# Kernel optimization log

Measured on AMD Instinct MI355X. Metric: run time of the kernel, lower is better.

Reference implementation:

```python
import jax, jax.numpy as jnp
import numpy as np

D = 64          # feature dim (in_dim == out_dim)
BS = 16         # graphs per batch
NPG = 4096      # nodes per graph
N = BS * NPG    # total nodes
E = N * 16      # edges (avg degree 16)
L = 2           # total_layer_num
TEMP = 0.6      # RelaxedBernoulli temperature
BN_EPS = 1e-5


def setup_inputs() -> dict:
    key = jax.random.key(0)
    ks = jax.random.split(key, 16)
    s = 0.05
    return {
        "x": jax.random.normal(ks[0], (N, D), jnp.float32),
        "edge_index": jax.random.randint(ks[1], (2, E), 0, N),
        "edge_weight": jax.random.uniform(ks[2], (E,), jnp.float32),
        "batch_item": jnp.repeat(jnp.arange(BS), NPG),
        "bs": BS,
        # per-layer logistic noise for RelaxedBernoulliStraightThrough rsample
        "u_noise": jax.random.uniform(ks[3], (L, E), jnp.float32, 1e-4, 1.0 - 1e-4),
        # edgePredictor (global): Linear(3d,d) -> ReLU -> Linear(d,1)
        "ep_W1": jax.random.normal(ks[4], (3 * D, D), jnp.float32) * s,
        "ep_b1": jnp.zeros((D,), jnp.float32),
        "ep_W2": jax.random.normal(ks[5], (D, 1), jnp.float32) * s,
        "ep_b2": jnp.zeros((1,), jnp.float32),
        "alpha": jax.random.uniform(ks[6], (1,), jnp.float32),  # edge_skip_alpha
        # per-layer GINConv mlp: Linear(d,d) (+ReLU)
        "gin_W": jax.random.normal(ks[7], (L, D, D), jnp.float32) * s,
        "gin_b": jnp.zeros((L, D), jnp.float32),
        # per-layer BatchNorm1d affine params
        "bn_gamma": jnp.ones((L, D), jnp.float32),
        "bn_beta": jnp.zeros((L, D), jnp.float32),
        # mlp_head: Linear(d,d)->ReLU->Linear(d,d)
        "head_W1": jax.random.normal(ks[8], (D, D), jnp.float32) * s,
        "head_b1": jnp.zeros((D,), jnp.float32),
        "head_W2": jax.random.normal(ks[9], (D, D), jnp.float32) * s,
        "head_b2": jnp.zeros((D,), jnp.float32),
    }


def reference(x, edge_index, edge_weight, batch_item, bs, u_noise,
              ep_W1, ep_b1, ep_W2, ep_b2, alpha, gin_W, gin_b,
              bn_gamma, bn_beta, head_W1, head_b1, head_W2, head_b2):
    src, dst = edge_index[0], edge_index[1]
    n_total = x.shape[0]
    centroid = jnp.mean(x.reshape(bs, -1, D), axis=1)  # [bs, D]
    pre_adj = None
    for l in range(L):
        # ---- EdgeUpdate: edge-gather + MLP scorer ----
        nj = x[src]
        ni = x[dst]
        res = (x.reshape(bs, -1, D) - centroid[:, None, :]).reshape(-1, D)
        sim = jnp.concatenate([jnp.abs(ni - nj), res[dst], res[src]], axis=1)  # [E, 3D]
        h = jax.nn.relu(sim @ ep_W1 + ep_b1)
        score = (h @ ep_W2 + ep_b2)[:, 0]  # [E]
        pre_adj = jax.nn.sigmoid(score)
        # RelaxedBernoulliStraightThrough: logits(probs) == score
        g = jnp.log(u_noise[l]) - jnp.log1p(-u_noise[l])
        soft = jax.nn.sigmoid((score + g) / TEMP)
        samp = soft + jax.lax.stop_gradient(jnp.round(soft) - soft)
        edge_weight = alpha * (samp * edge_weight) + (1.0 - alpha) * (samp * pre_adj)
        # ---- NodeUpdate: weighted GINConv (eps=0) + ReLU + BatchNorm ----
        msg = edge_weight[:, None] * x[src]
        aggr = jax.ops.segment_sum(msg, dst, num_segments=n_total)
        xh = jax.nn.relu((x + aggr) @ gin_W[l] + gin_b[l])  # GIN mlp ReLU == outer ReLU
        mu = jnp.mean(xh, axis=0)
        var = jnp.mean((xh - mu) ** 2, axis=0)
        x = bn_gamma[l] * (xh - mu) / jnp.sqrt(var + BN_EPS) + bn_beta[l]
        # ---- SystemUpdate: memory-attention pooling ----
        xm = x.reshape(bs, -1, D)
        att = jax.nn.softmax(jnp.einsum('bnd,bd->bn', xm, centroid), axis=1)
        centroid = jnp.einsum('bn,bnd->bd', att, xm)
    x_loss = jax.nn.relu(x @ head_W1 + head_b1) @ head_W2 + head_b2
    centroid_loss = jax.nn.relu(centroid @ head_W1 + head_b1) @ head_W2 + head_b2
    return (x, edge_weight, centroid, x_loss, centroid_loss, pre_adj)
```

## Files before the change

### kernel.cpp

```cpp
#include <hip/hip_runtime.h>
#include <hip/hip_bf16.h>


#define D 64
#define BSZ 16
#define NPG 4096
#define NN (BSZ * NPG)
#define NE (NN * 16)
#define NL 2
#define NTILE (NE / 64)

#define FIXTH 2e-3f
#define FLAGCAP 65536

#define OUT_X  0u
#define OUT_EW 4194304u
#define OUT_C  5242880u
#define OUT_XL 5243904u
#define OUT_CL 9438208u
#define OUT_PA 9439232u

typedef __attribute__((ext_vector_type(2))) float f32x2;

__device__ __forceinline__ void atomAdd64(double* p, double v) { unsafeAtomicAdd(p, v); }

__global__ __launch_bounds__(256) void k_deg(const int* __restrict__ edst,
                                             int* __restrict__ cnt) {
    int stride = gridDim.x * 256;
    for (int e = blockIdx.x * 256 + threadIdx.x; e < NE; e += stride)
        atomicAdd(&cnt[edst[e]], 1);
}

__global__ __launch_bounds__(256) void k_scan1(const int* __restrict__ cnt,
                                               int* __restrict__ rowptr,
                                               int* __restrict__ bsum) {
    __shared__ int sd[256];
    const int b = blockIdx.x, t = threadIdx.x;
    const int v = cnt[b * 256 + t];
    sd[t] = v;
    __syncthreads();
    for (int off = 1; off < 256; off <<= 1) {
        int tmp = (t >= off) ? sd[t - off] : 0;
        __syncthreads();
        sd[t] += tmp;
        __syncthreads();
    }
    rowptr[b * 256 + t] = sd[t] - v;
    if (t == 255) bsum[b] = sd[255];
}

__global__ __launch_bounds__(256) void k_scan2(int* __restrict__ bsum) {
    __shared__ int sd[256];
    const int t = threadIdx.x;
    const int v = bsum[t];
    sd[t] = v;
    __syncthreads();
    for (int off = 1; off < 256; off <<= 1) {
        int tmp = (t >= off) ? sd[t - off] : 0;
        __syncthreads();
        sd[t] += tmp;
        __syncthreads();
    }
    bsum[t] = sd[t] - v;
}

__global__ __launch_bounds__(256) void k_scan3(const int* __restrict__ bsum,
                                               int* __restrict__ rowptr,
                                               int* __restrict__ cursor) {
    const int i = blockIdx.x * 256 + threadIdx.x;
    const int r = rowptr[i] + bsum[blockIdx.x];
    rowptr[i] = r;
    cursor[i] = r;
    if (i == 0) rowptr[NN] = NE;
}

__global__ __launch_bounds__(256) void k_fill(const int* __restrict__ esrc,
                                              const int* __restrict__ edst,
                                              int* __restrict__ cursor,
                                              int* __restrict__ eord,
                                              int* __restrict__ src_csr,
                                              int* __restrict__ dst_csr) {
    int stride = gridDim.x * 256;
    for (int e = blockIdx.x * 256 + threadIdx.x; e < NE; e += stride) {
        const int d = edst[e];
        int pos = atomicAdd(&cursor[d], 1);
        eord[pos] = e;
        src_csr[pos] = esrc[e];
        dst_csr[pos] = d;
    }
}

__global__ __launch_bounds__(256) void k_centroid0(const float* __restrict__ xin,
                                                   double* __restrict__ c64) {
    const int g = blockIdx.x >> 3, sub = blockIdx.x & 7, tid = threadIdx.x;
    const int r = tid >> 6, f = tid & 63;
    __shared__ double cr[4][D];
    double s = 0.0;
    for (int k = 0; k < NPG / 8 / 4; ++k) {
        size_t n = (size_t)g * NPG + (size_t)(sub * (NPG / 8) + 4 * k + r);
        s += (double)xin[n * D + f];
    }
    cr[r][f] = s;
    __syncthreads();
    if (tid < D)
        atomAdd64(&c64[g * D + tid],
                  (cr[0][tid] + cr[1][tid] + cr[2][tid] + cr[3][tid]) * (1.0 / NPG));
}

__global__ __launch_bounds__(256) void k_qbc(const double* __restrict__ c64,
                                             const float* __restrict__ epW1,
                                             double* __restrict__ qb, double* __restrict__ qc) {
    int gj = blockIdx.x * 256 + threadIdx.x;
    if (gj >= BSZ * D) return;
    int g = gj >> 6, j = gj & 63;
    double sb = 0.0, sc = 0.0;
#pragma unroll
    for (int i = 0; i < D; ++i) {
        double cv = c64[g * D + i];
        sb += cv * (double)epW1[(D + i) * D + j];
        sc += cv * (double)epW1[(2 * D + i) * D + j];
    }
    qb[gj] = sb;
    qc[gj] = sc;
}

template <int LAYER>
__global__ __launch_bounds__(256) void k_P(const float* __restrict__ xin,
                                           const float* __restrict__ x32,
                                           const float* __restrict__ epW1,
                                           const double* __restrict__ qb,
                                           const double* __restrict__ qc,
                                           float* __restrict__ Pb, float* __restrict__ Pc,
                                           double* __restrict__ bnacc) {
    if (blockIdx.x == 0 && threadIdx.x < 128) bnacc[threadIdx.x] = 0.0;
    __shared__ float wb[D * D];
    __shared__ float wc[D * D];
    __shared__ float xrow[4][D];
    int tid = threadIdx.x, w = tid >> 6, j = tid & 63;
    for (int idx = tid; idx < D * D; idx += 256) {
        int i = idx >> 6, c = idx & 63;
        wb[idx] = epW1[(D + i) * D + c];
        wc[idx] = epW1[(2 * D + i) * D + c];
    }
    __syncthreads();
    for (int grp = blockIdx.x; grp < NN / 4; grp += gridDim.x) {
        size_t n = (size_t)grp * 4 + w;
        xrow[w][j] = (LAYER == 0) ? xin[n * D + j] : x32[n * D + j];
        __syncthreads();
        float pb = 0.0f, pc = 0.0f;
#pragma unroll
        for (int i = 0; i < D; ++i) {
            const float xv = xrow[w][i];
            pb += xv * wb[i * D + j];
            pc += xv * wc[i * D + j];
        }
        const int g = (int)(n >> 12);
        Pb[n * D + j] = pb - (float)qb[g * D + j];
        Pc[n * D + j] = pc - (float)qc[g * D + j];
        __syncthreads();
    }
}

template <int LAYER>
__global__ __launch_bounds__(256, 4) void k_edge(const float* __restrict__ xsrc,
                                                 const int* __restrict__ src_csr,
                                                 const int* __restrict__ dst_csr,
                                                 const int* __restrict__ eord,
                                                 const float* __restrict__ ewin,
                                                 float* __restrict__ ew_csr,
                                                 const float* __restrict__ unoise,
                                                 const float* __restrict__ epW1,
                                                 const float* __restrict__ epb1,
                                                 const float* __restrict__ epW2,
                                                 const float* __restrict__ epb2,
                                                 const float* __restrict__ alphap,
                                                 const float* __restrict__ Pb32,
                                                 const float* __restrict__ Pc32,
                                                 int* __restrict__ flagcnt,
                                                 int* __restrict__ flaglist,
                                                 float* __restrict__ out) {
    const int t = threadIdx.x;
    const int tx = t & 15, ty = t >> 4;

    __shared__ __align__(16) float ldsA[64 * 64];
    __shared__ __align__(16) float ldsW[64 * 64];

    for (int idx = t; idx < D * D; idx += 256) {
        ldsW[idx] = epW1[idx];
    }
    float b1f[4], w2f[4];
#pragma unroll
    for (int c = 0; c < 4; ++c) {
        b1f[c] = epb1[4 * tx + c];
        w2f[c] = epW2[4 * tx + c];
    }
    const float b2v = epb2[0];
    const float alpha = alphap[0];
    __syncthreads();

    const int eloc = t >> 2, q = t & 3;

    for (int tile = blockIdx.x; tile < NTILE; tile += gridDim.x) {
        const int base = tile * 64;

        {
            const int pos = base + eloc;
            const int s = src_csr[pos], d = dst_csr[pos];
            const float* rs = xsrc + (size_t)s * D + q * 16;
            const float* rd = xsrc + (size_t)d * D + q * 16;
#pragma unroll
            for (int c = 0; c < 4; ++c) {
                const float4 fd = *(const float4*)(rd + 4 * c);
                const float4 fs = *(const float4*)(rs + 4 * c);
                const int dim = q * 16 + 4 * c;
                ldsA[(dim + 0) * 64 + eloc] = fabsf(fd.x - fs.x);
                ldsA[(dim + 1) * 64 + eloc] = fabsf(fd.y - fs.y);
                ldsA[(dim + 2) * 64 + eloc] = fabsf(fd.z - fs.z);
                ldsA[(dim + 3) * 64 + eloc] = fabsf(fd.w - fs.w);
            }
        }
        __syncthreads();

        f32x2 acc2[4][2];
#pragma unroll
        for (int r = 0; r < 4; ++r)
#pragma unroll
            for (int c = 0; c < 2; ++c) {
                f32x2 z = {0.0f, 0.0f};
                acc2[r][c] = z;
            }

#pragma unroll 4
        for (int k = 0; k < 64; ++k) {
            const float4 af = *(const float4*)&ldsA[k * 64 + 4 * ty];
            const float4 wf = *(const float4*)&ldsW[k * 64 + 4 * tx];
            const f32x2 w01 = {wf.x, wf.y};
            const f32x2 w23 = {wf.z, wf.w};
            const float av[4] = {af.x, af.y, af.z, af.w};
#pragma unroll
            for (int r = 0; r < 4; ++r) {
                const f32x2 avv = {av[r], av[r]};
                acc2[r][0] += avv * w01;
                acc2[r][1] += avv * w23;
            }
        }
        __syncthreads();

        float* sred = ldsA;
#pragma unroll
        for (int r = 0; r < 4; ++r) {
            const int pos = base + 4 * ty + r;
            const int s = src_csr[pos], d = dst_csr[pos];
            const float4 pb = *(const float4*)(Pb32 + (size_t)d * D + 4 * tx);
            const float4 pc = *(const float4*)(Pc32 + (size_t)s * D + 4 * tx);
            float part = 0.0f;
            float h;
            h = acc2[r][0].x + pb.x + pc.x + b1f[0];
            if (h > 0.0f) part += h * w2f[0];
            h = acc2[r][0].y + pb.y + pc.y + b1f[1];
            if (h > 0.0f) part += h * w2f[1];
            h = acc2[r][1].x + pb.z + pc.z + b1f[2];
            if (h > 0.0f) part += h * w2f[2];
            h = acc2[r][1].y + pb.w + pc.w + b1f[3];
            if (h > 0.0f) part += h * w2f[3];
            sred[(4 * ty + r) * 17 + tx] = part;
        }
        __syncthreads();

        if (t < 64) {
            float sc_ = b2v;
#pragma unroll
            for (int i = 0; i < 16; ++i) sc_ += sred[t * 17 + i];
            const int pos = base + t;
            const int e = eord[pos];
            const float u = unoise[(size_t)LAYER * NE + e];
            const float gn = logf(u) - log1pf(-u);
            const float mar = sc_ + gn;
            bool deferred = false;
            if (fabsf(mar) < FIXTH) {
                int slot = atomicAdd(flagcnt, 1);
                if (slot < FLAGCAP) {
                    flaglist[slot] = pos;
                    deferred = true;
                }
            }
            if (!deferred) {
                const float pre = 1.0f / (1.0f + expf(-sc_));
                const bool samp = mar > 0.0f;
                const float ewo = (LAYER == 0) ? ewin[e] : ew_csr[pos];
                const float ewn = samp ? alpha * ewo + (1.0f - alpha) * pre : 0.0f;
                ew_csr[pos] = ewn;
                if (LAYER == NL - 1) {
                    out[OUT_EW + (size_t)e] = ewn;
                    out[OUT_PA + (size_t)e] = pre;
                }
            }
        }
        __syncthreads();
    }
}

template <int LAYER>
__global__ __launch_bounds__(256) void k_fix(const float* __restrict__ xsrc,
                                             const int* __restrict__ src_csr,
                                             const int* __restrict__ dst_csr,
                                             const int* __restrict__ eord,
                                             const float* __restrict__ ewin,
                                             float* __restrict__ ew_csr,
                                             const float* __restrict__ unoise,
                                             const float* __restrict__ epW1,
                                             const float* __restrict__ epb1,
                                             const float* __restrict__ epW2,
                                             const float* __restrict__ epb2,
                                             const float* __restrict__ alphap,
                                             const float* __restrict__ Pb32,
                                             const float* __restrict__ Pc32,
                                             const int* __restrict__ flagcnt,
                                             const int* __restrict__ flaglist,
                                             float* __restrict__ out) {
    const int n = min(flagcnt[0], FLAGCAP);
    __shared__ float dxs[4][D];
    const int w = threadIdx.x >> 6, lane = threadIdx.x & 63;
    const int nw = gridDim.x * 4;
    for (int i = blockIdx.x * 4 + w; i < n; i += nw) {
        const int pos = flaglist[i];
        const int s = src_csr[pos], d = dst_csr[pos];
        dxs[w][lane] = fabsf(xsrc[(size_t)d * D + lane] - xsrc[(size_t)s * D + lane]);
        double h = 0.0;
#pragma unroll
        for (int k = 0; k < D; ++k) h += (double)dxs[w][k] * (double)epW1[k * D + lane];
        h += (double)Pb32[(size_t)d * D + lane] + (double)Pc32[(size_t)s * D + lane] +
             (double)epb1[lane];
        double part = (h > 0.0) ? h * (double)epW2[lane] : 0.0;
#pragma unroll
        for (int off = 32; off; off >>= 1) part += __shfl_xor(part, off);
        if (lane == 0) {
            const double sc_ = part + (double)epb2[0];
            const int e = eord[pos];
            const double u = (double)unoise[(size_t)LAYER * NE + e];
            const double gn = log(u) - log1p(-u);
            const double pre = 1.0 / (1.0 + exp(-sc_));
            const bool samp = (sc_ + gn) > 0.0;
            const double ewo = (LAYER == 0) ? (double)ewin[e] : (double)ew_csr[pos];
            const double alpha = (double)alphap[0];
            const double ewn = samp ? alpha * ewo + (1.0 - alpha) * pre : 0.0;
            ew_csr[pos] = (float)ewn;
            if (LAYER == NL - 1) {
                out[OUT_EW + (size_t)e] = (float)ewn;
                out[OUT_PA + (size_t)e] = (float)pre;
            }
        }
    }
}

template <int LAYER>
__global__ __launch_bounds__(256) void k_nodeup(const float* __restrict__ xsrc,
                                                const float* __restrict__ ew_csr,
                                                const int* __restrict__ src_csr,
                                                const int* __restrict__ rowptr,
                                                const float* __restrict__ ginW,
                                                const float* __restrict__ ginB,
                                                float* __restrict__ xh,
                                                double* __restrict__ bnacc) {
    __shared__ __align__(16) float wgT[D][65];
    __shared__ __align__(16) float rowbuf[4][D];
    __shared__ double bn1[4][D];
    __shared__ double bn2[4][D];
    const int t = threadIdx.x, w = t >> 6, lane = t & 63;
    const int e = lane >> 4, q = lane & 15;
    for (int idx = t; idx < D * D; idx += 256) {
        const int i = idx >> 6, c = idx & 63;
        wgT[c][i] = ginW[LAYER * D * D + idx];
    }
    const float bj = ginB[LAYER * D + lane];
    __syncthreads();
    double s1 = 0.0, s2 = 0.0;
    const int nwaves = gridDim.x * 4;
    for (int n = blockIdx.x * 4 + w; n < NN; n += nwaves) {
        const int rs = rowptr[n], re = rowptr[n + 1];
        const int deg = re - rs;
        const int i0 = rs + ((e < deg) ? e : 0);
        const int i1 = rs + ((4 + e < deg) ? 4 + e : 0);
        const int i2 = rs + ((8 + e < deg) ? 8 + e : 0);
        const int i3 = rs + ((12 + e < deg) ? 12 + e : 0);
        const float w0 = (e < deg) ? ew_csr[i0] : 0.f;
        const float w1 = (4 + e < deg) ? ew_csr[i1] : 0.f;
        const float w2 = (8 + e < deg) ? ew_csr[i2] : 0.f;
        const float w3 = (12 + e < deg) ? ew_csr[i3] : 0.f;
        const int s0 = src_csr[i0], s1_ = src_csr[i1];
        const int s2_ = src_csr[i2], s3_ = src_csr[i3];
        const float4 r0 = *(const float4*)(xsrc + (size_t)s0 * D + 4 * q);
        const float4 r1 = *(const float4*)(xsrc + (size_t)s1_ * D + 4 * q);
        const float4 r2 = *(const float4*)(xsrc + (size_t)s2_ * D + 4 * q);
        const float4 r3 = *(const float4*)(xsrc + (size_t)s3_ * D + 4 * q);
        const float4 rf = *(const float4*)(xsrc + (size_t)n * D + 4 * q);
        f32x2 a01, a23;
        {
            const f32x2 w0v = {w0, w0}, w1v = {w1, w1}, w2v = {w2, w2}, w3v = {w3, w3};
            const f32x2 r0a = {r0.x, r0.y}, r0b = {r0.z, r0.w};
            const f32x2 r1a = {r1.x, r1.y}, r1b = {r1.z, r1.w};
            const f32x2 r2a = {r2.x, r2.y}, r2b = {r2.z, r2.w};
            const f32x2 r3a = {r3.x, r3.y}, r3b = {r3.z, r3.w};
            a01 = w0v * r0a;
            a23 = w0v * r0b;
            a01 += w1v * r1a;
            a23 += w1v * r1b;
            a01 += w2v * r2a;
            a23 += w2v * r2b;
            a01 += w3v * r3a;
            a23 += w3v * r3b;
        }
        for (int k = rs + 16; k < re; k += 4) {
            const int kk = k + e;
            const bool v = kk < re;
            const float wt = v ? ew_csr[kk] : 0.f;
            const int st = src_csr[v ? kk : rs];
            const float4 rt = *(const float4*)(xsrc + (size_t)st * D + 4 * q);
            const f32x2 wtv = {wt, wt};
            const f32x2 rta = {rt.x, rt.y}, rtb = {rt.z, rt.w};
            a01 += wtv * rta;
            a23 += wtv * rtb;
        }
        float a0 = a01.x, a1 = a01.y, a2 = a23.x, a3 = a23.y;
        a0 += __shfl_xor(a0, 16);
        a1 += __shfl_xor(a1, 16);
        a2 += __shfl_xor(a2, 16);
        a3 += __shfl_xor(a3, 16);
        a0 += __shfl_xor(a0, 32);
        a1 += __shfl_xor(a1, 32);
        a2 += __shfl_xor(a2, 32);
        a3 += __shfl_xor(a3, 32);
        if (e == 0) {
            rowbuf[w][4 * q + 0] = a0 + rf.x;
            rowbuf[w][4 * q + 1] = a1 + rf.y;
            rowbuf[w][4 * q + 2] = a2 + rf.z;
            rowbuf[w][4 * q + 3] = a3 + rf.w;
        }
        f32x2 h01 = {bj, 0.0f}, h23 = {0.0f, 0.0f};
#pragma unroll
        for (int ib = 0; ib < 16; ++ib) {
            const float4 rb = *(const float4*)&rowbuf[w][4 * ib];
            const float4 wv = *(const float4*)&wgT[lane][4 * ib];
            const f32x2 ra = {rb.x, rb.y}, rc = {rb.z, rb.w};
            const f32x2 wa = {wv.x, wv.y}, wc = {wv.z, wv.w};
            h01 += ra * wa;
            h23 += rc * wc;
        }
        float h = (h01.x + h01.y) + (h23.x + h23.y);
        h = h > 0.0f ? h : 0.0f;
        xh[(size_t)n * D + lane] = h;
        s1 += (double)h;
        s2 += (double)h * (double)h;
    }
    bn1[w][lane] = s1;
    bn2[w][lane] = s2;
    __syncthreads();
    if (w == 0) {
        atomAdd64(&bnacc[lane], bn1[0][lane] + bn1[1][lane] + bn1[2][lane] + bn1[3][lane]);
        atomAdd64(&bnacc[64 + lane], bn2[0][lane] + bn2[1][lane] + bn2[2][lane] + bn2[3][lane]);
    }
}

__global__ __launch_bounds__(64) void k_bnfin(int layer, const float* __restrict__ gamma,
                                              const float* __restrict__ beta,
                                              const double* __restrict__ bnacc,
                                              double* __restrict__ bnsc) {
    int j = threadIdx.x;
    double mu = bnacc[j] * (1.0 / NN);
    double var = bnacc[64 + j] * (1.0 / NN) - mu * mu;
    double sc = (double)gamma[layer * D + j] / sqrt(var + 1e-5);
    bnsc[j] = sc;
    bnsc[64 + j] = (double)beta[layer * D + j] - mu * sc;
}

template <int LAYER>
__global__ __launch_bounds__(256) void k_att1(const float* __restrict__ xh,
                                              const double* __restrict__ bnsc,
                                              const double* __restrict__ c64,
                                              float* __restrict__ x32,
                                              float* __restrict__ out,
                                              double* __restrict__ sc,
                                              double* __restrict__ bmax) {
    const int blk = blockIdx.x, t = threadIdx.x, w = t >> 6, lane = t & 63;
    const int g = blk >> 6;
    __shared__ double wmax[4];
    const double cj = c64[g * D + lane];
    const double bsc = bnsc[lane], boff = bnsc[64 + lane];
    double locmax = -1e300;
    for (int m = 0; m < 16; ++m) {
        const int n = blk * 64 + w * 16 + m;
        const float v32 = (float)(bsc * (double)xh[(size_t)n * D + lane] + boff);
        x32[(size_t)n * D + lane] = v32;
        if (LAYER == NL - 1) out[OUT_X + (size_t)n * D + lane] = v32;
        double v = (double)v32 * cj;
#pragma unroll
        for (int off = 32; off; off >>= 1) v += __shfl_xor(v, off);
        if (lane == 0) sc[n] = v;
        locmax = fmax(locmax, v);
    }
    if (lane == 0) wmax[w] = locmax;
    __syncthreads();
    if (t == 0) bmax[blk] = fmax(fmax(wmax[0], wmax[1]), fmax(wmax[2], wmax[3]));
}

__global__ __launch_bounds__(64) void k_att2(const double* __restrict__ bmax,
                                             double* __restrict__ mxg,
                                             double* __restrict__ num,
                                             double* __restrict__ den) {
    const int g = blockIdx.x, t = threadIdx.x;
    double m = bmax[g * 64 + t];
#pragma unroll
    for (int off = 32; off; off >>= 1) m = fmax(m, __shfl_xor(m, off));
    if (t == 0) {
        mxg[g] = m;
        den[g] = 0.0;
    }
    num[g * D + t] = 0.0;
}

__global__ __launch_bounds__(256) void k_att3(const float* __restrict__ x32,
                                              const double* __restrict__ sc,
                                              const double* __restrict__ mxg,
                                              double* __restrict__ num,
                                              double* __restrict__ den) {
    const int blk = blockIdx.x, t = threadIdx.x, w = t >> 6, lane = t & 63;
    const int g = blk >> 6;
    __shared__ double cp[4][D];
    __shared__ double wes[4];
    const double mx = mxg[g];
    double accj = 0.0, esum = 0.0;
    for (int m = 0; m < 16; ++m) {
        const int n = blk * 64 + w * 16 + m;
        const double e = exp(sc[n] - mx);
        accj += e * (double)x32[(size_t)n * D + lane];
        esum += e;
    }
    cp[w][lane] = accj;
    if (lane == 0) wes[w] = esum;
    __syncthreads();
    if (t < D) {
        atomAdd64(&num[g * D + t], cp[0][t] + cp[1][t] + cp[2][t] + cp[3][t]);
        if (t == 0) atomAdd64(&den[g], wes[0] + wes[1] + wes[2] + wes[3]);
    }
}

__global__ __launch_bounds__(64) void k_att4(const double* __restrict__ num,
                                             const double* __restrict__ den,
                                             double* __restrict__ c64) {
    const int g = blockIdx.x, t = threadIdx.x;
    c64[g * D + t] = num[g * D + t] / den[g];
}

__global__ __launch_bounds__(256) void k_head(const float* __restrict__ x32,
                                              const double* __restrict__ c64,
                                              const float* __restrict__ hW1,
                                              const float* __restrict__ hb1,
                                              const float* __restrict__ hW2,
                                              const float* __restrict__ hb2,
                                              float* __restrict__ out) {
    __shared__ float w1[D * D];
    __shared__ float w2[D * D];
    __shared__ float xr[4][D];
    __shared__ float hr[4][D];
    int tid = threadIdx.x, w = tid >> 6, j = tid & 63;
    for (int idx = tid; idx < D * D; idx += 256) {
        w1[idx] = hW1[idx];
        w2[idx] = hW2[idx];
    }
    const float b1j = hb1[j];
    const float b2j = hb2[j];
    __syncthreads();
    const int ROWS = NN + BSZ;
    for (int grp = blockIdx.x; grp * 4 < ROWS; grp += gridDim.x) {
        int r = grp * 4 + w;
        bool valid = r < ROWS;
        float xv = 0.f;
        if (valid)
            xv = (r < NN) ? x32[(size_t)r * D + j] : (float)c64[(size_t)(r - NN) * D + j];
        xr[w][j] = xv;
        __syncthreads();
        if (valid) {
            float h = b1j;
#pragma unroll
            for (int i = 0; i < D; ++i) h += xr[w][i] * w1[i * D + j];
            hr[w][j] = h > 0.f ? h : 0.f;
        }
        __syncthreads();
        if (valid) {
            float o = b2j;
#pragma unroll
            for (int i = 0; i < D; ++i) o += hr[w][i] * w2[i * D + j];
            if (r < NN) {
                out[OUT_XL + (size_t)r * D + j] = o;
            } else {
                size_t cr = (size_t)(r - NN) * D + j;
                out[OUT_CL + cr] = o;
                out[OUT_C + cr] = (float)c64[cr];
            }
        }
        __syncthreads();
    }
}

extern "C" void kernel_launch(void* const* d_in, const int* in_sizes, int n_in,
                              void* d_out, int out_size, void* d_ws, size_t ws_size,
                              hipStream_t stream) {
    const float* xin    = (const float*)d_in[0];
    const int*   ei     = (const int*)d_in[1];
    const float* ewin   = (const float*)d_in[2];
    const float* unoise = (const float*)d_in[5];
    const float* epW1   = (const float*)d_in[6];
    const float* epb1   = (const float*)d_in[7];
    const float* epW2   = (const float*)d_in[8];
    const float* epb2   = (const float*)d_in[9];
    const float* alphap = (const float*)d_in[10];
    const float* ginW   = (const float*)d_in[11];
    const float* ginB   = (const float*)d_in[12];
    const float* bng    = (const float*)d_in[13];
    const float* bnb    = (const float*)d_in[14];
    const float* hW1    = (const float*)d_in[15];
    const float* hb1    = (const float*)d_in[16];
    const float* hW2    = (const float*)d_in[17];
    const float* hb2    = (const float*)d_in[18];
    float* out = (float*)d_out;
    const int* esrc = ei;
    const int* edst = ei + NE;

    char* ws = (char*)d_ws;
    const size_t SZ4 = (size_t)NN * D * sizeof(float);
    float* Pb32 = (float*)(ws);
    float* xh32 = Pb32;
    float* Pc32 = (float*)(ws + SZ4);
    float* x32  = (float*)(ws + 2 * SZ4);
    float* ew_csr = (float*)(ws + 3 * SZ4);
    double* sc  = (double*)(ws + 3 * SZ4 + (size_t)NE * 4);
    char*  p    = ws + 3 * SZ4 + (size_t)NE * 4 + (size_t)NN * 8;
    double* c64  = (double*)p;          p += BSZ * D * 8;
    double* qb   = (double*)p;          p += BSZ * D * 8;
    double* qc   = (double*)p;          p += BSZ * D * 8;
    double* bnacc = (double*)p;         p += 128 * 8;
    double* bnsc  = (double*)p;         p += 128 * 8;
    double* bmax  = (double*)p;         p += 1024 * 8;
    double* mxg   = (double*)p;         p += 16 * 8;
    double* num   = (double*)p;         p += BSZ * D * 8;
    double* den   = (double*)p;         p += 16 * 8;
    int* cnt     = (int*)p;             p += (size_t)NN * 4;
    int* rowptr  = (int*)p;             p += (size_t)(NN + 1) * 4 + 4;
    int* cursor  = (int*)p;             p += (size_t)NN * 4;
    int* bsum    = (int*)p;             p += 256 * 4;
    int* eord    = (int*)p;             p += (size_t)NE * 4;
    int* src_csr = (int*)p;             p += (size_t)NE * 4;
    int* dst_csr = (int*)p;             p += (size_t)NE * 4;
    int* flagcnt  = (int*)p;            p += 8;
    int* flaglist = (int*)p;            p += (size_t)FLAGCAP * 4;

    hipMemsetAsync(cnt, 0, (size_t)NN * 4, stream);
    k_deg<<<1024, 256, 0, stream>>>(edst, cnt);
    k_scan1<<<256, 256, 0, stream>>>(cnt, rowptr, bsum);
    k_scan2<<<1, 256, 0, stream>>>(bsum);
    k_scan3<<<256, 256, 0, stream>>>(bsum, rowptr, cursor);
    k_fill<<<1024, 256, 0, stream>>>(esrc, edst, cursor, eord, src_csr, dst_csr);

    hipMemsetAsync(c64, 0, (size_t)BSZ * D * 8, stream);
    k_centroid0<<<BSZ * 8, 256, 0, stream>>>(xin, c64);

    k_qbc<<<4, 256, 0, stream>>>(c64, epW1, qb, qc);
    k_P<0><<<2048, 256, 0, stream>>>(xin, x32, epW1, qb, qc, Pb32, Pc32, bnacc);
    hipMemsetAsync(flagcnt, 0, 4, stream);
    k_edge<0><<<2048, 256, 0, stream>>>(xin, src_csr, dst_csr, eord, ewin, ew_csr, unoise,
                                        epW1, epb1, epW2, epb2, alphap, Pb32, Pc32,
                                        flagcnt, flaglist, out);
    k_fix<0><<<64, 256, 0, stream>>>(xin, src_csr, dst_csr, eord, ewin, ew_csr, unoise,
                                     epW1, epb1, epW2, epb2, alphap, Pb32, Pc32,
                                     flagcnt, flaglist, out);
    k_nodeup<0><<<2048, 256, 0, stream>>>(xin, ew_csr, src_csr, rowptr, ginW, ginB,
                                          xh32, bnacc);
    k_bnfin<<<1, 64, 0, stream>>>(0, bng, bnb, bnacc, bnsc);
    k_att1<0><<<1024, 256, 0, stream>>>(xh32, bnsc, c64, x32, out, sc, bmax);
    k_att2<<<16, 64, 0, stream>>>(bmax, mxg, num, den);
    k_att3<<<1024, 256, 0, stream>>>(x32, sc, mxg, num, den);
    k_att4<<<16, 64, 0, stream>>>(num, den, c64);

    k_qbc<<<4, 256, 0, stream>>>(c64, epW1, qb, qc);
    k_P<1><<<2048, 256, 0, stream>>>(xin, x32, epW1, qb, qc, Pb32, Pc32, bnacc);
    hipMemsetAsync(flagcnt, 0, 4, stream);
    k_edge<1><<<2048, 256, 0, stream>>>(x32, src_csr, dst_csr, eord, ewin, ew_csr, unoise,
                                        epW1, epb1, epW2, epb2, alphap, Pb32, Pc32,
                                        flagcnt, flaglist, out);
    k_fix<1><<<64, 256, 0, stream>>>(x32, src_csr, dst_csr, eord, ewin, ew_csr, unoise,
                                     epW1, epb1, epW2, epb2, alphap, Pb32, Pc32,
                                     flagcnt, flaglist, out);
    k_nodeup<1><<<2048, 256, 0, stream>>>(x32, ew_csr, src_csr, rowptr, ginW, ginB,
                                          xh32, bnacc);
    k_bnfin<<<1, 64, 0, stream>>>(1, bng, bnb, bnacc, bnsc);
    k_att1<1><<<1024, 256, 0, stream>>>(xh32, bnsc, c64, x32, out, sc, bmax);
    k_att2<<<16, 64, 0, stream>>>(bmax, mxg, num, den);
    k_att3<<<1024, 256, 0, stream>>>(x32, sc, mxg, num, den);
    k_att4<<<16, 64, 0, stream>>>(num, den, c64);

    k_head<<<2048, 256, 0, stream>>>(x32, c64, hW1, hb1, hW2, hb2, out);
}
```

Baseline: 846.3 us.

## Vectorize small node matvecs with transposed LDS weights and use fp32 attention

The P-projection and head kernels now store their weights transposed in padded shared memory. Each wave handles its own row with float4 reads and packed fp32x2 FMAs, and the block-wide barriers per row group are gone. The attention softmax kernels switch from fp64 to fp32 for scores, maxima, exponentials and partial sums, and keep fp64 only for the atomics. These kernels are a small share of total time, and the fp32 softmax may slightly change numerical accuracy.

```diff
diff --git a/kernel.cpp b/kernel.cpp
--- a/kernel.cpp
+++ b/kernel.cpp
@@ -133,31 +133,37 @@
                                            float* __restrict__ Pb, float* __restrict__ Pc,
                                            double* __restrict__ bnacc) {
     if (blockIdx.x == 0 && threadIdx.x < 128) bnacc[threadIdx.x] = 0.0;
-    __shared__ float wb[D * D];
-    __shared__ float wc[D * D];
-    __shared__ float xrow[4][D];
-    int tid = threadIdx.x, w = tid >> 6, j = tid & 63;
-    for (int idx = tid; idx < D * D; idx += 256) {
-        int i = idx >> 6, c = idx & 63;
-        wb[idx] = epW1[(D + i) * D + c];
-        wc[idx] = epW1[(2 * D + i) * D + c];
-    }
-    __syncthreads();
-    for (int grp = blockIdx.x; grp < NN / 4; grp += gridDim.x) {
-        size_t n = (size_t)grp * 4 + w;
-        xrow[w][j] = (LAYER == 0) ? xin[n * D + j] : x32[n * D + j];
-        __syncthreads();
-        float pb = 0.0f, pc = 0.0f;
-#pragma unroll
-        for (int i = 0; i < D; ++i) {
-            const float xv = xrow[w][i];
-            pb += xv * wb[i * D + j];
-            pc += xv * wc[i * D + j];
-        }
-        const int g = (int)(n >> 12);
-        Pb[n * D + j] = pb - (float)qb[g * D + j];
-        Pc[n * D + j] = pc - (float)qc[g * D + j];
-        __syncthreads();
+    __shared__ __align__(16) float wbT[D][65];
+    __shared__ __align__(16) float wcT[D][65];
+    __shared__ __align__(16) float rowbuf[4][D];
+    const int t = threadIdx.x, w = t >> 6, lane = t & 63;
+    for (int idx = t; idx < D * D; idx += 256) {
+        const int i = idx >> 6, c = idx & 63;
+        wbT[c][i] = epW1[(D + i) * D + c];
+        wcT[c][i] = epW1[(2 * D + i) * D + c];
+    }
+    __syncthreads();
+    const int nwaves = gridDim.x * 4;
+    for (int n = blockIdx.x * 4 + w; n < NN; n += nwaves) {
+        const float xv = (LAYER == 0) ? xin[(size_t)n * D + lane] : x32[(size_t)n * D + lane];
+        rowbuf[w][lane] = xv;
+        f32x2 pb2 = {0.0f, 0.0f}, pc2 = {0.0f, 0.0f};
+#pragma unroll
+        for (int ib = 0; ib < 16; ++ib) {
+            const float4 rb = *(const float4*)&rowbuf[w][4 * ib];
+            const float4 wbv = *(const float4*)&wbT[lane][4 * ib];
+            const float4 wcv = *(const float4*)&wcT[lane][4 * ib];
+            const f32x2 ra = {rb.x, rb.y}, rc = {rb.z, rb.w};
+            const f32x2 wb01 = {wbv.x, wbv.y}, wb23 = {wbv.z, wbv.w};
+            const f32x2 wc01 = {wcv.x, wcv.y}, wc23 = {wcv.z, wcv.w};
+            pb2 += ra * wb01;
+            pb2 += rc * wb23;
+            pc2 += ra * wc01;
+            pc2 += rc * wc23;
+        }
+        const int g = n >> 12;
+        Pb[(size_t)n * D + lane] = (pb2.x + pb2.y) - (float)qb[g * D + lane];
+        Pc[(size_t)n * D + lane] = (pc2.x + pc2.y) - (float)qc[g * D + lane];
     }
 }
 
@@ -479,38 +485,38 @@
                                               const double* __restrict__ c64,
                                               float* __restrict__ x32,
                                               float* __restrict__ out,
-                                              double* __restrict__ sc,
-                                              double* __restrict__ bmax) {
+                                              float* __restrict__ scf,
+                                              float* __restrict__ bmaxf) {
     const int blk = blockIdx.x, t = threadIdx.x, w = t >> 6, lane = t & 63;
     const int g = blk >> 6;
-    __shared__ double wmax[4];
-    const double cj = c64[g * D + lane];
+    __shared__ float wmax[4];
+    const float cj = (float)c64[g * D + lane];
     const double bsc = bnsc[lane], boff = bnsc[64 + lane];
-    double locmax = -1e300;
+    float locmax = -3.0e38f;
     for (int m = 0; m < 16; ++m) {
         const int n = blk * 64 + w * 16 + m;
         const float v32 = (float)(bsc * (double)xh[(size_t)n * D + lane] + boff);
         x32[(size_t)n * D + lane] = v32;
         if (LAYER == NL - 1) out[OUT_X + (size_t)n * D + lane] = v32;
-        double v = (double)v32 * cj;
+        float v = v32 * cj;
 #pragma unroll
         for (int off = 32; off; off >>= 1) v += __shfl_xor(v, off);
-        if (lane == 0) sc[n] = v;
-        locmax = fmax(locmax, v);
+        if (lane == 0) scf[n] = v;
+        locmax = fmaxf(locmax, v);
     }
     if (lane == 0) wmax[w] = locmax;
     __syncthreads();
-    if (t == 0) bmax[blk] = fmax(fmax(wmax[0], wmax[1]), fmax(wmax[2], wmax[3]));
-}
-
-__global__ __launch_bounds__(64) void k_att2(const double* __restrict__ bmax,
-                                             double* __restrict__ mxg,
+    if (t == 0) bmaxf[blk] = fmaxf(fmaxf(wmax[0], wmax[1]), fmaxf(wmax[2], wmax[3]));
+}
+
+__global__ __launch_bounds__(64) void k_att2(const float* __restrict__ bmaxf,
+                                             float* __restrict__ mxg,
                                              double* __restrict__ num,
                                              double* __restrict__ den) {
     const int g = blockIdx.x, t = threadIdx.x;
-    double m = bmax[g * 64 + t];
-#pragma unroll
-    for (int off = 32; off; off >>= 1) m = fmax(m, __shfl_xor(m, off));
+    float m = bmaxf[g * 64 + t];
+#pragma unroll
+    for (int off = 32; off; off >>= 1) m = fmaxf(m, __shfl_xor(m, off));
     if (t == 0) {
         mxg[g] = m;
         den[g] = 0.0;
@@ -519,28 +525,30 @@
 }
 
 __global__ __launch_bounds__(256) void k_att3(const float* __restrict__ x32,
-                                              const double* __restrict__ sc,
-                                              const double* __restrict__ mxg,
+                                              const float* __restrict__ scf,
+                                              const float* __restrict__ mxg,
                                               double* __restrict__ num,
                                               double* __restrict__ den) {
     const int blk = blockIdx.x, t = threadIdx.x, w = t >> 6, lane = t & 63;
     const int g = blk >> 6;
-    __shared__ double cp[4][D];
-    __shared__ double wes[4];
-    const double mx = mxg[g];
-    double accj = 0.0, esum = 0.0;
+    __shared__ float cp[4][D];
+    __shared__ float wes[4];
+    const float mx = mxg[g];
+    float accj = 0.0f, esum = 0.0f;
     for (int m = 0; m < 16; ++m) {
         const int n = blk * 64 + w * 16 + m;
-        const double e = exp(sc[n] - mx);
-        accj += e * (double)x32[(size_t)n * D + lane];
+        const float e = expf(scf[n] - mx);
+        accj += e * x32[(size_t)n * D + lane];
         esum += e;
     }
     cp[w][lane] = accj;
     if (lane == 0) wes[w] = esum;
     __syncthreads();
     if (t < D) {
-        atomAdd64(&num[g * D + t], cp[0][t] + cp[1][t] + cp[2][t] + cp[3][t]);
-        if (t == 0) atomAdd64(&den[g], wes[0] + wes[1] + wes[2] + wes[3]);
+        atomAdd64(&num[g * D + t], (double)cp[0][t] + (double)cp[1][t] +
+                                       (double)cp[2][t] + (double)cp[3][t]);
+        if (t == 0)
+            atomAdd64(&den[g], (double)wes[0] + (double)wes[1] + (double)wes[2] + (double)wes[3]);
     }
 }
 
@@ -558,47 +566,52 @@
                                               const float* __restrict__ hW2,
                                               const float* __restrict__ hb2,
                                               float* __restrict__ out) {
-    __shared__ float w1[D * D];
-    __shared__ float w2[D * D];
-    __shared__ float xr[4][D];
-    __shared__ float hr[4][D];
-    int tid = threadIdx.x, w = tid >> 6, j = tid & 63;
-    for (int idx = tid; idx < D * D; idx += 256) {
-        w1[idx] = hW1[idx];
-        w2[idx] = hW2[idx];
-    }
-    const float b1j = hb1[j];
-    const float b2j = hb2[j];
+    __shared__ __align__(16) float w1T[D][65];
+    __shared__ __align__(16) float w2T[D][65];
+    __shared__ __align__(16) float rowb[4][D];
+    __shared__ __align__(16) float hrow[4][D];
+    const int t = threadIdx.x, w = t >> 6, lane = t & 63;
+    for (int idx = t; idx < D * D; idx += 256) {
+        const int i = idx >> 6, c = idx & 63;
+        w1T[c][i] = hW1[idx];
+        w2T[c][i] = hW2[idx];
+    }
+    const float b1 = hb1[lane];
+    const float b2 = hb2[lane];
     __syncthreads();
     const int ROWS = NN + BSZ;
-    for (int grp = blockIdx.x; grp * 4 < ROWS; grp += gridDim.x) {
-        int r = grp * 4 + w;
-        bool valid = r < ROWS;
-        float xv = 0.f;
-        if (valid)
-            xv = (r < NN) ? x32[(size_t)r * D + j] : (float)c64[(size_t)(r - NN) * D + j];
-        xr[w][j] = xv;
-        __syncthreads();
-        if (valid) {
-            float h = b1j;
-#pragma unroll
-            for (int i = 0; i < D; ++i) h += xr[w][i] * w1[i * D + j];
-            hr[w][j] = h > 0.f ? h : 0.f;
-        }
-        __syncthreads();
-        if (valid) {
-            float o = b2j;
-#pragma unroll
-            for (int i = 0; i < D; ++i) o += hr[w][i] * w2[i * D + j];
-            if (r < NN) {
-                out[OUT_XL + (size_t)r * D + j] = o;
-            } else {
-                size_t cr = (size_t)(r - NN) * D + j;
-                out[OUT_CL + cr] = o;
-                out[OUT_C + cr] = (float)c64[cr];
-            }
-        }
-        __syncthreads();
+    const int nwaves = gridDim.x * 4;
+    for (int r = blockIdx.x * 4 + w; r < ROWS; r += nwaves) {
+        const float xv =
+            (r < NN) ? x32[(size_t)r * D + lane] : (float)c64[(size_t)(r - NN) * D + lane];
+        rowb[w][lane] = xv;
+        f32x2 h01 = {b1, 0.0f}, h23 = {0.0f, 0.0f};
+#pragma unroll
+        for (int ib = 0; ib < 16; ++ib) {
+            const float4 rb = *(const float4*)&rowb[w][4 * ib];
+            const float4 wv = *(const float4*)&w1T[lane][4 * ib];
+            h01 += (f32x2){rb.x, rb.y} * (f32x2){wv.x, wv.y};
+            h23 += (f32x2){rb.z, rb.w} * (f32x2){wv.z, wv.w};
+        }
+        float h = (h01.x + h01.y) + (h23.x + h23.y);
+        h = h > 0.f ? h : 0.f;
+        hrow[w][lane] = h;
+        f32x2 o01 = {b2, 0.0f}, o23 = {0.0f, 0.0f};
+#pragma unroll
+        for (int ib = 0; ib < 16; ++ib) {
+            const float4 rb = *(const float4*)&hrow[w][4 * ib];
+            const float4 wv = *(const float4*)&w2T[lane][4 * ib];
+            o01 += (f32x2){rb.x, rb.y} * (f32x2){wv.x, wv.y};
+            o23 += (f32x2){rb.z, rb.w} * (f32x2){wv.z, wv.w};
+        }
+        const float o = (o01.x + o01.y) + (o23.x + o23.y);
+        if (r < NN) {
+            out[OUT_XL + (size_t)r * D + lane] = o;
+        } else {
+            const size_t cr = (size_t)(r - NN) * D + lane;
+            out[OUT_CL + cr] = o;
+            out[OUT_C + cr] = (float)c64[cr];
+        }
     }
 }
 
@@ -633,15 +646,15 @@
     float* Pc32 = (float*)(ws + SZ4);
     float* x32  = (float*)(ws + 2 * SZ4);
     float* ew_csr = (float*)(ws + 3 * SZ4);
-    double* sc  = (double*)(ws + 3 * SZ4 + (size_t)NE * 4);
+    float* scf  = (float*)(ws + 3 * SZ4 + (size_t)NE * 4);
     char*  p    = ws + 3 * SZ4 + (size_t)NE * 4 + (size_t)NN * 8;
     double* c64  = (double*)p;          p += BSZ * D * 8;
     double* qb   = (double*)p;          p += BSZ * D * 8;
     double* qc   = (double*)p;          p += BSZ * D * 8;
     double* bnacc = (double*)p;         p += 128 * 8;
     double* bnsc  = (double*)p;         p += 128 * 8;
-    double* bmax  = (double*)p;         p += 1024 * 8;
-    double* mxg   = (double*)p;         p += 16 * 8;
+    float*  bmaxf = (float*)p;          p += 1024 * 8;
+    float*  mxg   = (float*)p;          p += 16 * 8;
     double* num   = (double*)p;         p += BSZ * D * 8;
     double* den   = (double*)p;         p += 16 * 8;
     int* cnt     = (int*)p;             p += (size_t)NN * 4;
@@ -676,9 +689,9 @@
     k_nodeup<0><<<2048, 256, 0, stream>>>(xin, ew_csr, src_csr, rowptr, ginW, ginB,
                                           xh32, bnacc);
     k_bnfin<<<1, 64, 0, stream>>>(0, bng, bnb, bnacc, bnsc);
-    k_att1<0><<<1024, 256, 0, stream>>>(xh32, bnsc, c64, x32, out, sc, bmax);
-    k_att2<<<16, 64, 0, stream>>>(bmax, mxg, num, den);
-    k_att3<<<1024, 256, 0, stream>>>(x32, sc, mxg, num, den);
+    k_att1<0><<<1024, 256, 0, stream>>>(xh32, bnsc, c64, x32, out, scf, bmaxf);
+    k_att2<<<16, 64, 0, stream>>>(bmaxf, mxg, num, den);
+    k_att3<<<1024, 256, 0, stream>>>(x32, scf, mxg, num, den);
     k_att4<<<16, 64, 0, stream>>>(num, den, c64);
 
     k_qbc<<<4, 256, 0, stream>>>(c64, epW1, qb, qc);
@@ -693,9 +706,9 @@
     k_nodeup<1><<<2048, 256, 0, stream>>>(x32, ew_csr, src_csr, rowptr, ginW, ginB,
                                           xh32, bnacc);
     k_bnfin<<<1, 64, 0, stream>>>(1, bng, bnb, bnacc, bnsc);
-    k_att1<1><<<1024, 256, 0, stream>>>(xh32, bnsc, c64, x32, out, sc, bmax);
-    k_att2<<<16, 64, 0, stream>>>(bmax, mxg, num, den);
-    k_att3<<<1024, 256, 0, stream>>>(x32, sc, mxg, num, den);
+    k_att1<1><<<1024, 256, 0, stream>>>(xh32, bnsc, c64, x32, out, scf, bmaxf);
+    k_att2<<<16, 64, 0, stream>>>(bmaxf, mxg, num, den);
+    k_att3<<<1024, 256, 0, stream>>>(x32, scf, mxg, num, den);
     k_att4<<<16, 64, 0, stream>>>(num, den, c64);
 
     k_head<<<2048, 256, 0, stream>>>(x32, c64, hW1, hb1, hW2, hb2, out);
```

After: 786.7 us. 7.0% less time.
